# Performance work log

Measured on AMD Instinct MI355X. Metric: run time of the kernel, lower is better.

Reference implementation:

```python
import jax, jax.numpy as jnp
import numpy as np

N = 50000   # nodes
E = 800000  # edges
D = 256     # input feature dim
H = 128     # hidden size
OUT = 40    # output classes


def setup_inputs() -> dict:
    key = jax.random.key(0)
    ks = jax.random.split(key, 10)
    s = 0.05
    return {
        "x": jax.random.normal(ks[0], (N, D), jnp.float32),
        "edge_index": jax.random.randint(ks[1], (2, E), 0, N, dtype=jnp.int64),
        "W0": jax.random.normal(ks[2], (D, H), jnp.float32) * s,
        "b0": jnp.zeros((H,), jnp.float32),
        "W1": jax.random.normal(ks[3], (H, H), jnp.float32) * s,
        "b1": jnp.zeros((H,), jnp.float32),
        "W2": jax.random.normal(ks[4], (H, H), jnp.float32) * s,
        "b2": jnp.zeros((H,), jnp.float32),
        "Wout": jax.random.normal(ks[5], (H * 3, OUT), jnp.float32) * s,
        "bout": jnp.zeros((OUT,), jnp.float32),
    }


def _gcn_norm(edge_index, n):
    # PyG gcn_norm: add self-loops, symmetric D^-1/2 (A+I) D^-1/2 weights
    row, col = edge_index[0], edge_index[1]
    loop = jnp.arange(n, dtype=edge_index.dtype)
    row = jnp.concatenate([row, loop])
    col = jnp.concatenate([col, loop])
    deg = jax.ops.segment_sum(jnp.ones_like(col, jnp.float32), col, num_segments=n)
    dinv = jnp.where(deg > 0, jax.lax.rsqrt(jnp.maximum(deg, 1.0)), 0.0)
    norm = dinv[row] * dinv[col]  # [E+N]
    return row, col, norm


def _gcn_conv(x, W, b, row, col, norm, n):
    h = x @ W                                   # dense transform first (PyG order)
    msg = h[row] * norm[:, None]                # gather source feats, scale
    out = jax.ops.segment_sum(msg, col, num_segments=n)  # scatter-aggregate
    return out + b


def reference(x, edge_index, W0, b0, W1, b1, W2, b2, Wout, bout):
    n = x.shape[0]
    row, col, norm = _gcn_norm(edge_index, n)
    x1 = jax.nn.relu(_gcn_conv(x, W0, b0, row, col, norm, n))
    x2 = jax.nn.relu(_gcn_conv(x1, W1, b1, row, col, norm, n))
    x3 = jax.nn.relu(_gcn_conv(x2, W2, b2, row, col, norm, n))
    xs = jnp.concatenate([x1, x2, x3], axis=-1)  # JumpingKnowledge 'cat'
    return xs @ Wout + bout
```

## Files before the change

kernel.cpp:

```cpp
#include <hip/hip_runtime.h>

#define HID 128
#define NOUT 40
#define SCAN_B 256
#define NWIN 8

typedef __attribute__((ext_vector_type(8))) short bf16x8;
typedef __attribute__((ext_vector_type(4))) float f32x4;

__device__ inline float bf2f(unsigned int u) {
    unsigned int t = u << 16;
    float f;
    __builtin_memcpy(&f, &t, 4);
    return f;
}
__device__ inline unsigned short f2bf(float f) {
    unsigned int x;
    __builtin_memcpy(&x, &f, 4);
    unsigned int r = (x + 0x7fffu + ((x >> 16) & 1u)) >> 16;
    return (unsigned short)r;
}
__device__ inline bf16x8 pack_bf8(float4 u, float4 v) {
    bf16x8 r;
    r[0] = (short)f2bf(u.x); r[1] = (short)f2bf(u.y);
    r[2] = (short)f2bf(u.z); r[3] = (short)f2bf(u.w);
    r[4] = (short)f2bf(v.x); r[5] = (short)f2bf(v.y);
    r[6] = (short)f2bf(v.z); r[7] = (short)f2bf(v.w);
    return r;
}

__global__ void prep_kernel(const unsigned int* __restrict__ e, int* __restrict__ flag,
                            int* __restrict__ deg, int N) {
    if (blockIdx.x == 0 && threadIdx.x < 64) {
        unsigned int v = e[2 * threadIdx.x + 1];
        unsigned long long ball = __ballot(v == 0u);
        if (threadIdx.x == 0) *flag = (ball == ~0ull) ? 1 : 0;
    }
    int stride = gridDim.x * blockDim.x;
    for (int j = blockIdx.x * blockDim.x + threadIdx.x; j < N; j += stride) deg[j] = 0;
}

__global__ void degwt_kernel(const void* __restrict__ eix, const int* __restrict__ flag,
                             int* __restrict__ deg, int E, int gE,
                             const float* __restrict__ W0, const float* __restrict__ W1,
                             const float* __restrict__ W2, const float* __restrict__ Wo,
                             unsigned short* __restrict__ W0t, unsigned short* __restrict__ W1t,
                             unsigned short* __restrict__ W2t, unsigned short* __restrict__ Wot) {
    if (blockIdx.x < gE) {
        int i = blockIdx.x * blockDim.x + threadIdx.x;
        if (i >= E) return;
        int f = *flag;
        int c = f ? (int)(((const long long*)eix)[(size_t)E + i]) : ((const int*)eix)[(size_t)E + i];
        atomicAdd(&deg[c], 1);
    } else {
        int idx = (blockIdx.x - gE) * blockDim.x + threadIdx.x;
        const int s0 = 128 * 256, s1 = 128 * 128, s2 = 128 * 128, s3 = 48 * 384;
        if (idx < s0) {
            int n = idx >> 8, k = idx & 255;
            W0t[idx] = f2bf(W0[(size_t)k * 128 + n]);
        } else if ((idx -= s0) < s1) {
            int n = idx >> 7, k = idx & 127;
            W1t[idx] = f2bf(W1[(size_t)k * 128 + n]);
        } else if ((idx -= s1) < s2) {
            int n = idx >> 7, k = idx & 127;
            W2t[idx] = f2bf(W2[(size_t)k * 128 + n]);
        } else if ((idx -= s2) < s3) {
            int n = idx / 384, k = idx - n * 384;
            Wot[idx] = (n < NOUT) ? f2bf(Wo[(size_t)k * NOUT + n]) : (unsigned short)0;
        }
    }
}

__global__ void scan1_kernel(const int* __restrict__ deg, int* __restrict__ offs,
                             int* __restrict__ bsum, float* __restrict__ dinv, int N) {
    __shared__ int s[SCAN_B];
    int i = blockIdx.x * SCAN_B + threadIdx.x;
    int v = (i < N) ? deg[i] : 0;
    if (i < N) dinv[i] = rsqrtf((float)v + 1.0f);
    s[threadIdx.x] = v;
    __syncthreads();
    for (int d = 1; d < SCAN_B; d <<= 1) {
        int t = (threadIdx.x >= d) ? s[threadIdx.x - d] : 0;
        __syncthreads();
        s[threadIdx.x] += t;
        __syncthreads();
    }
    if (i < N) offs[i] = s[threadIdx.x] - v;
    if (threadIdx.x == SCAN_B - 1) bsum[blockIdx.x] = s[SCAN_B - 1];
}

__global__ void scan2_kernel(int* __restrict__ bsum, int nb) {
    __shared__ int s[SCAN_B];
    int v = (threadIdx.x < nb) ? bsum[threadIdx.x] : 0;
    s[threadIdx.x] = v;
    __syncthreads();
    for (int d = 1; d < SCAN_B; d <<= 1) {
        int t = (threadIdx.x >= d) ? s[threadIdx.x - d] : 0;
        __syncthreads();
        s[threadIdx.x] += t;
        __syncthreads();
    }
    if (threadIdx.x < nb) bsum[threadIdx.x] = s[threadIdx.x] - v;
}

__global__ void scan3_kernel(int* __restrict__ offs, const int* __restrict__ bsum,
                             int* __restrict__ cursor, int N, int E) {
    int i = blockIdx.x * SCAN_B + threadIdx.x;
    if (i < N) {
        int v = offs[i] + bsum[blockIdx.x];
        offs[i] = v;
        cursor[i] = v;
    }
    if (blockIdx.x == 0 && threadIdx.x == 0) offs[N] = E;
}

__global__ __launch_bounds__(256) void fill_csr_kernel(
    const void* __restrict__ eix, const int* __restrict__ flag,
    const float* __restrict__ dinv, int* __restrict__ cursor,
    int2* __restrict__ pkd, int E, int N) {
    const int wn = blockIdx.x & (NWIN - 1);
    const int slice = blockIdx.x >> 3;
    const int nslice = gridDim.x >> 3;
    const int wsz = (N + NWIN - 1) / NWIN;
    const int lo = wn * wsz, hi = lo + wsz;
    const int f = *flag;
    const int stride = nslice * 256;
    for (int i = slice * 256 + threadIdx.x; i < E; i += stride) {
        int r, c;
        if (f) {
            r = (int)(((const long long*)eix)[i]);
            c = (int)(((const long long*)eix)[(size_t)E + i]);
        } else {
            r = ((const int*)eix)[i];
            c = ((const int*)eix)[(size_t)E + i];
        }
        if (c >= lo && c < hi) {
            int p = atomicAdd(&cursor[c], 1);
            int2 rec;
            rec.x = r;
            rec.y = __float_as_int(dinv[r] * dinv[c]);
            pkd[p] = rec;
        }
    }
}

template <bool AF32, int K>
__global__ __launch_bounds__(256) void gemm_mfma_kernel(
    const void* __restrict__ Ap, const unsigned short* __restrict__ Wt,
    unsigned short* __restrict__ H, int M) {
    __shared__ unsigned short Bs[128 * 128];
    const int tid = threadIdx.x;
    const int lane = tid & 63;
    const int w = tid >> 6;
    const int lr = lane & 15;
    const int ko = lane >> 4;
    const int bm = blockIdx.x * 128;

    f32x4 acc[2][8];
#pragma unroll
    for (int i = 0; i < 2; ++i)
#pragma unroll
        for (int j = 0; j < 8; ++j) acc[i][j] = (f32x4){0.f, 0.f, 0.f, 0.f};

    size_t aoff[2];
#pragma unroll
    for (int mi = 0; mi < 2; ++mi) {
        int R = bm + w * 32 + mi * 16 + lr;
        if (R >= M) R = M - 1;
        aoff[mi] = (size_t)R * K + ko * 8;
    }

#pragma unroll
    for (int kp = 0; kp < K; kp += 128) {
        for (int c = tid; c < 128 * 16; c += 256) {
            int row = c >> 4;
            int ch = c & 15;
            int sch = ch ^ (row & 7);
            *(bf16x8*)(Bs + row * 128 + sch * 8) =
                *(const bf16x8*)(Wt + (size_t)row * K + kp + ch * 8);
        }
        __syncthreads();

#pragma unroll
        for (int k0 = 0; k0 < 128; k0 += 32) {
            bf16x8 a[2], b[8];
#pragma unroll
            for (int mi = 0; mi < 2; ++mi) {
                if constexpr (AF32) {
                    const float* p = (const float*)Ap + aoff[mi] + kp + k0;
                    float4 u = *(const float4*)p;
                    float4 v = *(const float4*)(p + 4);
                    a[mi] = pack_bf8(u, v);
                } else {
                    a[mi] = *(const bf16x8*)((const unsigned short*)Ap + aoff[mi] + kp + k0);
                }
            }
            const int chb = (k0 >> 3) + ko;
#pragma unroll
            for (int ni = 0; ni < 8; ++ni) {
                int row = ni * 16 + lr;
                b[ni] = *(const bf16x8*)(Bs + row * 128 + ((chb ^ (row & 7)) * 8));
            }
#pragma unroll
            for (int mi = 0; mi < 2; ++mi)
#pragma unroll
                for (int ni = 0; ni < 8; ++ni)
                    acc[mi][ni] = __builtin_amdgcn_mfma_f32_16x16x32_bf16(a[mi], b[ni], acc[mi][ni], 0, 0, 0);
        }
        __syncthreads();
    }

    unsigned short* Cw = Bs + w * (16 * 136);
#pragma unroll
    for (int mi = 0; mi < 2; ++mi) {
#pragma unroll
        for (int ni = 0; ni < 8; ++ni)
#pragma unroll
            for (int r = 0; r < 4; ++r)
                Cw[(ko * 4 + r) * 136 + ni * 16 + lr] = f2bf(acc[mi][ni][r]);
        const int R0 = bm + w * 32 + mi * 16;
#pragma unroll
        for (int p = 0; p < 4; ++p) {
            int row = p * 4 + (lane >> 4);
            int col = (lane & 15) * 8;
            int Ro = R0 + row;
            if (Ro < M) {
                uint4 v = *(const uint4*)(Cw + row * 136 + col);
                *(uint4*)(H + (size_t)Ro * HID + col) = v;
            }
        }
    }
}

__global__ __launch_bounds__(256) void agg_csr_kernel(
    const unsigned int* __restrict__ h32, const int* __restrict__ offs,
    const int2* __restrict__ pkd, const float* __restrict__ dinv,
    const float* __restrict__ bias, unsigned int* __restrict__ xo, int N) {
    const int lane = threadIdx.x & 63;
    const int n = (blockIdx.x * blockDim.x + threadIdx.x) >> 6;
    if (n >= N) return;
    const float d = dinv[n];
    unsigned int sv = h32[(size_t)n * 64 + lane];
    float ax = bf2f(sv & 0xffff) * (d * d) + bias[2 * lane + 0];
    float ay = bf2f(sv >> 16) * (d * d) + bias[2 * lane + 1];
    int e = offs[n];
    const int e1 = offs[n + 1];

    for (; e + 16 <= e1; e += 16) {
        int2 pk[16];
        unsigned int v[16];
#pragma unroll
        for (int j = 0; j < 16; ++j) pk[j] = pkd[e + j];
#pragma unroll
        for (int j = 0; j < 16; ++j) v[j] = h32[(size_t)pk[j].x * 64 + lane];
#pragma unroll
        for (int j = 0; j < 16; ++j) {
            float wv = __int_as_float(pk[j].y);
            ax += bf2f(v[j] & 0xffff) * wv;
            ay += bf2f(v[j] >> 16) * wv;
        }
    }
    for (; e + 4 <= e1; e += 4) {
        int2 pk[4];
        unsigned int v[4];
#pragma unroll
        for (int j = 0; j < 4; ++j) pk[j] = pkd[e + j];
#pragma unroll
        for (int j = 0; j < 4; ++j) v[j] = h32[(size_t)pk[j].x * 64 + lane];
#pragma unroll
        for (int j = 0; j < 4; ++j) {
            float wv = __int_as_float(pk[j].y);
            ax += bf2f(v[j] & 0xffff) * wv;
            ay += bf2f(v[j] >> 16) * wv;
        }
    }
    for (; e < e1; ++e) {
        int2 pk = pkd[e];
        unsigned int v = h32[(size_t)pk.x * 64 + lane];
        float wv = __int_as_float(pk.y);
        ax += bf2f(v & 0xffff) * wv;
        ay += bf2f(v >> 16) * wv;
    }
    ax = fmaxf(ax, 0.f);
    ay = fmaxf(ay, 0.f);
    xo[(size_t)n * 64 + lane] = (unsigned int)f2bf(ax) | ((unsigned int)f2bf(ay) << 16);
}

__global__ __launch_bounds__(256) void head_mfma_kernel(
    const unsigned short* __restrict__ x1, const unsigned short* __restrict__ x2,
    const unsigned short* __restrict__ x3, const unsigned short* __restrict__ Wt,
    const float* __restrict__ bout, float* __restrict__ out, int M) {
    const int tid = threadIdx.x;
    const int lane = tid & 63;
    const int w = tid >> 6;
    const int lr = lane & 15;
    const int ko = lane >> 4;
    const int bm = blockIdx.x * 64;
    int R = bm + w * 16 + lr;
    if (R >= M) R = M - 1;
    const unsigned short* xs[3] = {x1, x2, x3};

    f32x4 acc[3];
#pragma unroll
    for (int i = 0; i < 3; ++i) acc[i] = (f32x4){0.f, 0.f, 0.f, 0.f};

#pragma unroll
    for (int s = 0; s < 3; ++s) {
        const unsigned short* xp = xs[s] + (size_t)R * HID + ko * 8;
#pragma unroll
        for (int c = 0; c < 4; ++c) {
            bf16x8 a = *(const bf16x8*)(xp + c * 32);
#pragma unroll
            for (int ni = 0; ni < 3; ++ni) {
                bf16x8 b = *(const bf16x8*)(Wt + (size_t)(ni * 16 + lr) * 384 + s * 128 + c * 32 + ko * 8);
                acc[ni] = __builtin_amdgcn_mfma_f32_16x16x32_bf16(a, b, acc[ni], 0, 0, 0);
            }
        }
    }

    int Rb = bm + w * 16 + ko * 4;
#pragma unroll
    for (int r = 0; r < 4; ++r) {
        int Ro = Rb + r;
        if (Ro < M) {
#pragma unroll
            for (int ni = 0; ni < 3; ++ni) {
                int C = ni * 16 + lr;
                if (C < NOUT) out[(size_t)Ro * NOUT + C] = acc[ni][r] + bout[C];
            }
        }
    }
}

static inline size_t align_up(size_t x, size_t a) { return (x + a - 1) / a * a; }

extern "C" void kernel_launch(void* const* d_in, const int* in_sizes, int n_in,
                              void* d_out, int out_size, void* d_ws, size_t ws_size,
                              hipStream_t stream) {
    const float* x    = (const float*)d_in[0];
    const void*  eix  = d_in[1];
    const float* W0   = (const float*)d_in[2];
    const float* b0   = (const float*)d_in[3];
    const float* W1   = (const float*)d_in[4];
    const float* b1   = (const float*)d_in[5];
    const float* W2   = (const float*)d_in[6];
    const float* b2   = (const float*)d_in[7];
    const float* Wout = (const float*)d_in[8];
    const float* bout = (const float*)d_in[9];
    float* out = (float*)d_out;

    const int D = 256;
    const int N = in_sizes[0] / D;
    const int E = in_sizes[1] / 2;

    char* w = (char*)d_ws;
    size_t off = 0;
    int* deg = (int*)(w + off);             off = align_up(off + (size_t)N * 4, 256);
    float* dinv = (float*)(w + off);        off = align_up(off + (size_t)N * 4, 256);
    int* offs = (int*)(w + off);            off = align_up(off + (size_t)(N + 1) * 4, 256);
    int* cursor = (int*)(w + off);          off = align_up(off + (size_t)N * 4, 256);
    int* bsum = (int*)(w + off);            off = align_up(off + 1024 * 4, 256);
    int* flag = (int*)(w + off);            off = align_up(off + 16, 256);
    int2* pkd = (int2*)(w + off);           off = align_up(off + (size_t)E * 8, 256);
    unsigned short* h   = (unsigned short*)(w + off); off = align_up(off + (size_t)N * HID * 2, 256);
    unsigned short* x1b = (unsigned short*)(w + off); off = align_up(off + (size_t)N * HID * 2, 256);
    unsigned short* x2b = (unsigned short*)(w + off); off = align_up(off + (size_t)N * HID * 2, 256);
    unsigned short* x3b = (unsigned short*)(w + off); off = align_up(off + (size_t)N * HID * 2, 256);
    unsigned short* W0t = (unsigned short*)(w + off); off = align_up(off + (size_t)HID * 256 * 2, 256);
    unsigned short* W1t = (unsigned short*)(w + off); off = align_up(off + (size_t)HID * HID * 2, 256);
    unsigned short* W2t = (unsigned short*)(w + off); off = align_up(off + (size_t)HID * HID * 2, 256);
    unsigned short* Wot = (unsigned short*)(w + off); off = align_up(off + (size_t)48 * 384 * 2, 256);
    (void)ws_size;

    prep_kernel<<<128, 256, 0, stream>>>((const unsigned int*)eix, flag, deg, N);

    const int gE = (E + 255) / 256;
    const int wtTot = 128 * 256 + 128 * 128 + 128 * 128 + 48 * 384;
    const int gW = (wtTot + 255) / 256;
    degwt_kernel<<<gE + gW, 256, 0, stream>>>(eix, flag, deg, E, gE,
                                              W0, W1, W2, Wout, W0t, W1t, W2t, Wot);

    const int nb = (N + SCAN_B - 1) / SCAN_B;
    scan1_kernel<<<nb, SCAN_B, 0, stream>>>(deg, offs, bsum, dinv, N);
    scan2_kernel<<<1, SCAN_B, 0, stream>>>(bsum, nb);
    scan3_kernel<<<nb, SCAN_B, 0, stream>>>(offs, bsum, cursor, N, E);
    fill_csr_kernel<<<NWIN * 256, 256, 0, stream>>>(eix, flag, dinv, cursor, pkd, E, N);

    const int gGemm = (N + 127) / 128;
    const int gAgg = (N * 64 + 255) / 256;

    gemm_mfma_kernel<true, 256><<<gGemm, 256, 0, stream>>>(x, W0t, h, N);
    agg_csr_kernel<<<gAgg, 256, 0, stream>>>((const unsigned int*)h, offs, pkd, dinv, b0, (unsigned int*)x1b, N);
    gemm_mfma_kernel<false, 128><<<gGemm, 256, 0, stream>>>(x1b, W1t, h, N);
    agg_csr_kernel<<<gAgg, 256, 0, stream>>>((const unsigned int*)h, offs, pkd, dinv, b1, (unsigned int*)x2b, N);
    gemm_mfma_kernel<false, 128><<<gGemm, 256, 0, stream>>>(x2b, W2t, h, N);
    agg_csr_kernel<<<gAgg, 256, 0, stream>>>((const unsigned int*)h, offs, pkd, dinv, b2, (unsigned int*)x3b, N);
    head_mfma_kernel<<<(N + 63) / 64, 256, 0, stream>>>(x1b, x2b, x3b, Wot, bout, out, N);
}
```

Before: 359.7 us.

## Fuse CSR fill with first GEMM and merge scan passes

Merges the second and third scan kernels into one, with each block re-scanning the block sums locally, and fuses the CSR fill kernel with the first-layer GEMM into a single launch that splits work by block index. This removes two launches and lets the independent edge-fill and dense transform run concurrently on the GPU. The cost is that fill blocks now reserve the GEMM's shared memory, which can reduce occupancy for the atomic scatter, and the two workloads compete for resources.

```diff
diff --git a/kernel.cpp b/kernel.cpp
--- a/kernel.cpp
+++ b/kernel.cpp
@@ -4,6 +4,7 @@
 #define NOUT 40
 #define SCAN_B 256
 #define NWIN 8
+#define FILLB (NWIN * 256)
 
 typedef __attribute__((ext_vector_type(8))) short bf16x8;
 typedef __attribute__((ext_vector_type(4))) float f32x4;
@@ -89,7 +90,8 @@
     if (threadIdx.x == SCAN_B - 1) bsum[blockIdx.x] = s[SCAN_B - 1];
 }
 
-__global__ void scan2_kernel(int* __restrict__ bsum, int nb) {
+__global__ void scan23_kernel(int* __restrict__ offs, const int* __restrict__ bsum,
+                              int* __restrict__ cursor, int N, int E, int nb) {
     __shared__ int s[SCAN_B];
     int v = (threadIdx.x < nb) ? bsum[threadIdx.x] : 0;
     s[threadIdx.x] = v;
@@ -100,53 +102,135 @@
         s[threadIdx.x] += t;
         __syncthreads();
     }
-    if (threadIdx.x < nb) bsum[threadIdx.x] = s[threadIdx.x] - v;
-}
-
-__global__ void scan3_kernel(int* __restrict__ offs, const int* __restrict__ bsum,
-                             int* __restrict__ cursor, int N, int E) {
+    const int base = (blockIdx.x == 0) ? 0 : s[blockIdx.x - 1];
     int i = blockIdx.x * SCAN_B + threadIdx.x;
     if (i < N) {
-        int v = offs[i] + bsum[blockIdx.x];
-        offs[i] = v;
-        cursor[i] = v;
+        int o = offs[i] + base;
+        offs[i] = o;
+        cursor[i] = o;
     }
     if (blockIdx.x == 0 && threadIdx.x == 0) offs[N] = E;
 }
 
-__global__ __launch_bounds__(256) void fill_csr_kernel(
+__global__ __launch_bounds__(256) void fillgemm0_kernel(
     const void* __restrict__ eix, const int* __restrict__ flag,
     const float* __restrict__ dinv, int* __restrict__ cursor,
-    int2* __restrict__ pkd, int E, int N) {
-    const int wn = blockIdx.x & (NWIN - 1);
-    const int slice = blockIdx.x >> 3;
-    const int nslice = gridDim.x >> 3;
-    const int wsz = (N + NWIN - 1) / NWIN;
-    const int lo = wn * wsz, hi = lo + wsz;
-    const int f = *flag;
-    const int stride = nslice * 256;
-    for (int i = slice * 256 + threadIdx.x; i < E; i += stride) {
-        int r, c;
-        if (f) {
-            r = (int)(((const long long*)eix)[i]);
-            c = (int)(((const long long*)eix)[(size_t)E + i]);
-        } else {
-            r = ((const int*)eix)[i];
-            c = ((const int*)eix)[(size_t)E + i];
-        }
-        if (c >= lo && c < hi) {
-            int p = atomicAdd(&cursor[c], 1);
-            int2 rec;
-            rec.x = r;
-            rec.y = __float_as_int(dinv[r] * dinv[c]);
-            pkd[p] = rec;
-        }
-    }
-}
-
-template <bool AF32, int K>
+    int2* __restrict__ pkd, int E, int N,
+    const float* __restrict__ Ap, const unsigned short* __restrict__ Wt,
+    unsigned short* __restrict__ H, int M) {
+    __shared__ unsigned short Bs[128 * 128];
+    const int tid = threadIdx.x;
+
+    if (blockIdx.x < FILLB) {
+        const int wn = blockIdx.x & (NWIN - 1);
+        const int slice = blockIdx.x >> 3;
+        const int nslice = FILLB >> 3;
+        const int wsz = (N + NWIN - 1) / NWIN;
+        const int lo = wn * wsz, hi = lo + wsz;
+        const int f = *flag;
+        const int stride = nslice * 256;
+        for (int i = slice * 256 + tid; i < E; i += stride) {
+            int r, c;
+            if (f) {
+                r = (int)(((const long long*)eix)[i]);
+                c = (int)(((const long long*)eix)[(size_t)E + i]);
+            } else {
+                r = ((const int*)eix)[i];
+                c = ((const int*)eix)[(size_t)E + i];
+            }
+            if (c >= lo && c < hi) {
+                int p = atomicAdd(&cursor[c], 1);
+                int2 rec;
+                rec.x = r;
+                rec.y = __float_as_int(dinv[r] * dinv[c]);
+                pkd[p] = rec;
+            }
+        }
+        return;
+    }
+
+    constexpr int K = 256;
+    const int lane = tid & 63;
+    const int w = tid >> 6;
+    const int lr = lane & 15;
+    const int ko = lane >> 4;
+    const int bm = (blockIdx.x - FILLB) * 128;
+
+    f32x4 acc[2][8];
+#pragma unroll
+    for (int i = 0; i < 2; ++i)
+#pragma unroll
+        for (int j = 0; j < 8; ++j) acc[i][j] = (f32x4){0.f, 0.f, 0.f, 0.f};
+
+    size_t aoff[2];
+#pragma unroll
+    for (int mi = 0; mi < 2; ++mi) {
+        int R = bm + w * 32 + mi * 16 + lr;
+        if (R >= M) R = M - 1;
+        aoff[mi] = (size_t)R * K + ko * 8;
+    }
+
+#pragma unroll
+    for (int kp = 0; kp < K; kp += 128) {
+        for (int c = tid; c < 128 * 16; c += 256) {
+            int row = c >> 4;
+            int ch = c & 15;
+            int sch = ch ^ (row & 7);
+            *(bf16x8*)(Bs + row * 128 + sch * 8) =
+                *(const bf16x8*)(Wt + (size_t)row * K + kp + ch * 8);
+        }
+        __syncthreads();
+
+#pragma unroll
+        for (int k0 = 0; k0 < 128; k0 += 32) {
+            bf16x8 a[2], b[8];
+#pragma unroll
+            for (int mi = 0; mi < 2; ++mi) {
+                const float* p = Ap + aoff[mi] + kp + k0;
+                float4 u = *(const float4*)p;
+                float4 v = *(const float4*)(p + 4);
+                a[mi] = pack_bf8(u, v);
+            }
+            const int chb = (k0 >> 3) + ko;
+#pragma unroll
+            for (int ni = 0; ni < 8; ++ni) {
+                int row = ni * 16 + lr;
+                b[ni] = *(const bf16x8*)(Bs + row * 128 + ((chb ^ (row & 7)) * 8));
+            }
+#pragma unroll
+            for (int mi = 0; mi < 2; ++mi)
+#pragma unroll
+                for (int ni = 0; ni < 8; ++ni)
+                    acc[mi][ni] = __builtin_amdgcn_mfma_f32_16x16x32_bf16(a[mi], b[ni], acc[mi][ni], 0, 0, 0);
+        }
+        __syncthreads();
+    }
+
+    unsigned short* Cw = Bs + w * (16 * 136);
+#pragma unroll
+    for (int mi = 0; mi < 2; ++mi) {
+#pragma unroll
+        for (int ni = 0; ni < 8; ++ni)
+#pragma unroll
+            for (int r = 0; r < 4; ++r)
+                Cw[(ko * 4 + r) * 136 + ni * 16 + lr] = f2bf(acc[mi][ni][r]);
+        const int R0 = bm + w * 32 + mi * 16;
+#pragma unroll
+        for (int p = 0; p < 4; ++p) {
+            int row = p * 4 + (lane >> 4);
+            int col = (lane & 15) * 8;
+            int Ro = R0 + row;
+            if (Ro < M) {
+                uint4 v = *(const uint4*)(Cw + row * 136 + col);
+                *(uint4*)(H + (size_t)Ro * HID + col) = v;
+            }
+        }
+    }
+}
+
+template <int K>
 __global__ __launch_bounds__(256) void gemm_mfma_kernel(
-    const void* __restrict__ Ap, const unsigned short* __restrict__ Wt,
+    const unsigned short* __restrict__ Ap, const unsigned short* __restrict__ Wt,
     unsigned short* __restrict__ H, int M) {
     __shared__ unsigned short Bs[128 * 128];
     const int tid = threadIdx.x;
@@ -185,16 +269,8 @@
         for (int k0 = 0; k0 < 128; k0 += 32) {
             bf16x8 a[2], b[8];
 #pragma unroll
-            for (int mi = 0; mi < 2; ++mi) {
-                if constexpr (AF32) {
-                    const float* p = (const float*)Ap + aoff[mi] + kp + k0;
-                    float4 u = *(const float4*)p;
-                    float4 v = *(const float4*)(p + 4);
-                    a[mi] = pack_bf8(u, v);
-                } else {
-                    a[mi] = *(const bf16x8*)((const unsigned short*)Ap + aoff[mi] + kp + k0);
-                }
-            }
+            for (int mi = 0; mi < 2; ++mi)
+                a[mi] = *(const bf16x8*)(Ap + aoff[mi] + kp + k0);
             const int chb = (k0 >> 3) + ko;
 #pragma unroll
             for (int ni = 0; ni < 8; ++ni) {
@@ -382,18 +458,17 @@
 
     const int nb = (N + SCAN_B - 1) / SCAN_B;
     scan1_kernel<<<nb, SCAN_B, 0, stream>>>(deg, offs, bsum, dinv, N);
-    scan2_kernel<<<1, SCAN_B, 0, stream>>>(bsum, nb);
-    scan3_kernel<<<nb, SCAN_B, 0, stream>>>(offs, bsum, cursor, N, E);
-    fill_csr_kernel<<<NWIN * 256, 256, 0, stream>>>(eix, flag, dinv, cursor, pkd, E, N);
+    scan23_kernel<<<nb, SCAN_B, 0, stream>>>(offs, bsum, cursor, N, E, nb);
 
     const int gGemm = (N + 127) / 128;
     const int gAgg = (N * 64 + 255) / 256;
 
-    gemm_mfma_kernel<true, 256><<<gGemm, 256, 0, stream>>>(x, W0t, h, N);
+    fillgemm0_kernel<<<FILLB + gGemm, 256, 0, stream>>>(eix, flag, dinv, cursor, pkd, E, N,
+                                                        x, W0t, h, N);
     agg_csr_kernel<<<gAgg, 256, 0, stream>>>((const unsigned int*)h, offs, pkd, dinv, b0, (unsigned int*)x1b, N);
-    gemm_mfma_kernel<false, 128><<<gGemm, 256, 0, stream>>>(x1b, W1t, h, N);
+    gemm_mfma_kernel<128><<<gGemm, 256, 0, stream>>>(x1b, W1t, h, N);
     agg_csr_kernel<<<gAgg, 256, 0, stream>>>((const unsigned int*)h, offs, pkd, dinv, b1, (unsigned int*)x2b, N);
-    gemm_mfma_kernel<false, 128><<<gGemm, 256, 0, stream>>>(x2b, W2t, h, N);
+    gemm_mfma_kernel<128><<<gGemm, 256, 0, stream>>>(x2b, W2t, h, N);
     agg_csr_kernel<<<gAgg, 256, 0, stream>>>((const unsigned int*)h, offs, pkd, dinv, b2, (unsigned int*)x3b, N);
     head_mfma_kernel<<<(N + 63) / 64, 256, 0, stream>>>(x1b, x2b, x3b, Wot, bout, out, N);
 }
```

After: 360.1 us. No clear change (+0.1%).

## Merge all GCN stages into one cooperative persistent kernel with grid syncs

Applied to the files above, without the earlier changes.

Replaces the chain of separate kernels (prep, degree, scans, CSR fill, three GEMM+aggregate layers, head) with a single cooperative mega-kernel that walks through each stage using grid-stride loops and separates them with grid-wide barriers. The grid is sized from occupancy, assuming 256 CUs and capped at 2048 blocks. The aim is to remove the per-launch overhead and the idle gaps between the many small kernels. In exchange every stage runs at a fixed persistent grid, pays grid-barrier costs, and loses per-kernel register and occupancy tuning. The GEMM staging stride also moves from 136 to 144.

```diff
diff --git a/kernel.cpp b/kernel.cpp
--- a/kernel.cpp
+++ b/kernel.cpp
@@ -1,8 +1,10 @@
 #include <hip/hip_runtime.h>
+#include <hip/hip_cooperative_groups.h>
+
+namespace cg = cooperative_groups;
 
 #define HID 128
 #define NOUT 40
-#define SCAN_B 256
 #define NWIN 8
 
 typedef __attribute__((ext_vector_type(8))) short bf16x8;
@@ -29,304 +31,324 @@
     return r;
 }
 
-__global__ void prep_kernel(const unsigned int* __restrict__ e, int* __restrict__ flag,
-                            int* __restrict__ deg, int N) {
-    if (blockIdx.x == 0 && threadIdx.x < 64) {
-        unsigned int v = e[2 * threadIdx.x + 1];
-        unsigned long long ball = __ballot(v == 0u);
-        if (threadIdx.x == 0) *flag = (ball == ~0ull) ? 1 : 0;
-    }
-    int stride = gridDim.x * blockDim.x;
-    for (int j = blockIdx.x * blockDim.x + threadIdx.x; j < N; j += stride) deg[j] = 0;
-}
-
-__global__ void degwt_kernel(const void* __restrict__ eix, const int* __restrict__ flag,
-                             int* __restrict__ deg, int E, int gE,
-                             const float* __restrict__ W0, const float* __restrict__ W1,
-                             const float* __restrict__ W2, const float* __restrict__ Wo,
-                             unsigned short* __restrict__ W0t, unsigned short* __restrict__ W1t,
-                             unsigned short* __restrict__ W2t, unsigned short* __restrict__ Wot) {
-    if (blockIdx.x < gE) {
-        int i = blockIdx.x * blockDim.x + threadIdx.x;
-        if (i >= E) return;
-        int f = *flag;
-        int c = f ? (int)(((const long long*)eix)[(size_t)E + i]) : ((const int*)eix)[(size_t)E + i];
-        atomicAdd(&deg[c], 1);
-    } else {
-        int idx = (blockIdx.x - gE) * blockDim.x + threadIdx.x;
-        const int s0 = 128 * 256, s1 = 128 * 128, s2 = 128 * 128, s3 = 48 * 384;
-        if (idx < s0) {
-            int n = idx >> 8, k = idx & 255;
-            W0t[idx] = f2bf(W0[(size_t)k * 128 + n]);
-        } else if ((idx -= s0) < s1) {
-            int n = idx >> 7, k = idx & 127;
-            W1t[idx] = f2bf(W1[(size_t)k * 128 + n]);
-        } else if ((idx -= s1) < s2) {
-            int n = idx >> 7, k = idx & 127;
-            W2t[idx] = f2bf(W2[(size_t)k * 128 + n]);
-        } else if ((idx -= s2) < s3) {
-            int n = idx / 384, k = idx - n * 384;
-            Wot[idx] = (n < NOUT) ? f2bf(Wo[(size_t)k * NOUT + n]) : (unsigned short)0;
-        }
-    }
-}
-
-__global__ void scan1_kernel(const int* __restrict__ deg, int* __restrict__ offs,
-                             int* __restrict__ bsum, float* __restrict__ dinv, int N) {
-    __shared__ int s[SCAN_B];
-    int i = blockIdx.x * SCAN_B + threadIdx.x;
-    int v = (i < N) ? deg[i] : 0;
-    if (i < N) dinv[i] = rsqrtf((float)v + 1.0f);
-    s[threadIdx.x] = v;
-    __syncthreads();
-    for (int d = 1; d < SCAN_B; d <<= 1) {
-        int t = (threadIdx.x >= d) ? s[threadIdx.x - d] : 0;
-        __syncthreads();
-        s[threadIdx.x] += t;
-        __syncthreads();
-    }
-    if (i < N) offs[i] = s[threadIdx.x] - v;
-    if (threadIdx.x == SCAN_B - 1) bsum[blockIdx.x] = s[SCAN_B - 1];
-}
-
-__global__ void scan2_kernel(int* __restrict__ bsum, int nb) {
-    __shared__ int s[SCAN_B];
-    int v = (threadIdx.x < nb) ? bsum[threadIdx.x] : 0;
-    s[threadIdx.x] = v;
-    __syncthreads();
-    for (int d = 1; d < SCAN_B; d <<= 1) {
-        int t = (threadIdx.x >= d) ? s[threadIdx.x - d] : 0;
-        __syncthreads();
-        s[threadIdx.x] += t;
-        __syncthreads();
-    }
-    if (threadIdx.x < nb) bsum[threadIdx.x] = s[threadIdx.x] - v;
-}
-
-__global__ void scan3_kernel(int* __restrict__ offs, const int* __restrict__ bsum,
-                             int* __restrict__ cursor, int N, int E) {
-    int i = blockIdx.x * SCAN_B + threadIdx.x;
-    if (i < N) {
-        int v = offs[i] + bsum[blockIdx.x];
-        offs[i] = v;
-        cursor[i] = v;
-    }
-    if (blockIdx.x == 0 && threadIdx.x == 0) offs[N] = E;
-}
-
-__global__ __launch_bounds__(256) void fill_csr_kernel(
-    const void* __restrict__ eix, const int* __restrict__ flag,
-    const float* __restrict__ dinv, int* __restrict__ cursor,
-    int2* __restrict__ pkd, int E, int N) {
-    const int wn = blockIdx.x & (NWIN - 1);
-    const int slice = blockIdx.x >> 3;
-    const int nslice = gridDim.x >> 3;
-    const int wsz = (N + NWIN - 1) / NWIN;
-    const int lo = wn * wsz, hi = lo + wsz;
-    const int f = *flag;
-    const int stride = nslice * 256;
-    for (int i = slice * 256 + threadIdx.x; i < E; i += stride) {
-        int r, c;
-        if (f) {
-            r = (int)(((const long long*)eix)[i]);
-            c = (int)(((const long long*)eix)[(size_t)E + i]);
-        } else {
-            r = ((const int*)eix)[i];
-            c = ((const int*)eix)[(size_t)E + i];
-        }
-        if (c >= lo && c < hi) {
-            int p = atomicAdd(&cursor[c], 1);
-            int2 rec;
-            rec.x = r;
-            rec.y = __float_as_int(dinv[r] * dinv[c]);
-            pkd[p] = rec;
-        }
-    }
-}
+struct MP {
+    const void* eix;
+    const float* x;
+    const float *W0, *b0, *W1, *b1, *W2, *b2, *Wo, *bo;
+    float* out;
+    int *deg, *offs, *cursor, *bsum, *flag;
+    float* dinv;
+    int2* pkd;
+    unsigned short *h, *x1, *x2, *x3, *W0t, *W1t, *W2t, *Wot;
+    int N, E;
+};
 
 template <bool AF32, int K>
-__global__ __launch_bounds__(256) void gemm_mfma_kernel(
-    const void* __restrict__ Ap, const unsigned short* __restrict__ Wt,
-    unsigned short* __restrict__ H, int M) {
-    __shared__ unsigned short Bs[128 * 128];
+__device__ inline void gemm_phase(const void* Ap, const unsigned short* Wt,
+                                  unsigned short* H, int M, unsigned short* Bs, int G) {
     const int tid = threadIdx.x;
     const int lane = tid & 63;
     const int w = tid >> 6;
     const int lr = lane & 15;
     const int ko = lane >> 4;
-    const int bm = blockIdx.x * 128;
-
-    f32x4 acc[2][8];
-#pragma unroll
-    for (int i = 0; i < 2; ++i)
-#pragma unroll
-        for (int j = 0; j < 8; ++j) acc[i][j] = (f32x4){0.f, 0.f, 0.f, 0.f};
-
-    size_t aoff[2];
-#pragma unroll
-    for (int mi = 0; mi < 2; ++mi) {
-        int R = bm + w * 32 + mi * 16 + lr;
-        if (R >= M) R = M - 1;
-        aoff[mi] = (size_t)R * K + ko * 8;
-    }
-
-#pragma unroll
-    for (int kp = 0; kp < K; kp += 128) {
-        for (int c = tid; c < 128 * 16; c += 256) {
-            int row = c >> 4;
-            int ch = c & 15;
-            int sch = ch ^ (row & 7);
-            *(bf16x8*)(Bs + row * 128 + sch * 8) =
-                *(const bf16x8*)(Wt + (size_t)row * K + kp + ch * 8);
-        }
+    const int nt = (M + 127) >> 7;
+
+    for (int t = blockIdx.x; t < nt; t += G) {
+        const int bm = t << 7;
+        f32x4 acc[2][8];
+#pragma unroll
+        for (int i = 0; i < 2; ++i)
+#pragma unroll
+            for (int j = 0; j < 8; ++j) acc[i][j] = (f32x4){0.f, 0.f, 0.f, 0.f};
+
+        size_t aoff[2];
+#pragma unroll
+        for (int mi = 0; mi < 2; ++mi) {
+            int R = bm + w * 32 + mi * 16 + lr;
+            if (R >= M) R = M - 1;
+            aoff[mi] = (size_t)R * K + ko * 8;
+        }
+
         __syncthreads();
-
-#pragma unroll
-        for (int k0 = 0; k0 < 128; k0 += 32) {
-            bf16x8 a[2], b[8];
-#pragma unroll
-            for (int mi = 0; mi < 2; ++mi) {
-                if constexpr (AF32) {
-                    const float* p = (const float*)Ap + aoff[mi] + kp + k0;
-                    float4 u = *(const float4*)p;
-                    float4 v = *(const float4*)(p + 4);
-                    a[mi] = pack_bf8(u, v);
-                } else {
-                    a[mi] = *(const bf16x8*)((const unsigned short*)Ap + aoff[mi] + kp + k0);
+#pragma unroll
+        for (int kp = 0; kp < K; kp += 128) {
+            for (int c = tid; c < 128 * 16; c += 256) {
+                int row = c >> 4;
+                int ch = c & 15;
+                int sch = ch ^ (row & 7);
+                *(bf16x8*)(Bs + row * 128 + sch * 8) =
+                    *(const bf16x8*)(Wt + (size_t)row * K + kp + ch * 8);
+            }
+            __syncthreads();
+#pragma unroll
+            for (int k0 = 0; k0 < 128; k0 += 32) {
+                bf16x8 a[2], b[8];
+#pragma unroll
+                for (int mi = 0; mi < 2; ++mi) {
+                    if constexpr (AF32) {
+                        const float* p = (const float*)Ap + aoff[mi] + kp + k0;
+                        float4 u = *(const float4*)p;
+                        float4 v = *(const float4*)(p + 4);
+                        a[mi] = pack_bf8(u, v);
+                    } else {
+                        a[mi] = *(const bf16x8*)((const unsigned short*)Ap + aoff[mi] + kp + k0);
+                    }
                 }
-            }
-            const int chb = (k0 >> 3) + ko;
-#pragma unroll
-            for (int ni = 0; ni < 8; ++ni) {
-                int row = ni * 16 + lr;
-                b[ni] = *(const bf16x8*)(Bs + row * 128 + ((chb ^ (row & 7)) * 8));
-            }
-#pragma unroll
-            for (int mi = 0; mi < 2; ++mi)
-#pragma unroll
-                for (int ni = 0; ni < 8; ++ni)
-                    acc[mi][ni] = __builtin_amdgcn_mfma_f32_16x16x32_bf16(a[mi], b[ni], acc[mi][ni], 0, 0, 0);
-        }
+                const int chb = (k0 >> 3) + ko;
+#pragma unroll
+                for (int ni = 0; ni < 8; ++ni) {
+                    int row = ni * 16 + lr;
+                    b[ni] = *(const bf16x8*)(Bs + row * 128 + ((chb ^ (row & 7)) * 8));
+                }
+#pragma unroll
+                for (int mi = 0; mi < 2; ++mi)
+#pragma unroll
+                    for (int ni = 0; ni < 8; ++ni)
+                        acc[mi][ni] = __builtin_amdgcn_mfma_f32_16x16x32_bf16(a[mi], b[ni], acc[mi][ni], 0, 0, 0);
+            }
+            __syncthreads();
+        }
+
+        unsigned short* Cw = Bs + w * (16 * 144);
+#pragma unroll
+        for (int mi = 0; mi < 2; ++mi) {
+#pragma unroll
+            for (int ni = 0; ni < 8; ++ni)
+#pragma unroll
+                for (int r = 0; r < 4; ++r)
+                    Cw[(ko * 4 + r) * 144 + ni * 16 + lr] = f2bf(acc[mi][ni][r]);
+            const int R0 = bm + w * 32 + mi * 16;
+#pragma unroll
+            for (int p = 0; p < 4; ++p) {
+                int row = p * 4 + (lane >> 4);
+                int col = (lane & 15) * 8;
+                int Ro = R0 + row;
+                if (Ro < M) {
+                    uint4 v = *(const uint4*)(Cw + row * 144 + col);
+                    *(uint4*)(H + (size_t)Ro * HID + col) = v;
+                }
+            }
+        }
+    }
+}
+
+__device__ inline void agg_phase(const unsigned int* __restrict__ h32, const int* __restrict__ offs,
+                                 const int2* __restrict__ pkd, const float* __restrict__ dinv,
+                                 const float* __restrict__ bias, unsigned int* __restrict__ xo,
+                                 int N, int G) {
+    const int lane = threadIdx.x & 63;
+    const int nw = G * 4;
+    for (int n = ((blockIdx.x * 256 + threadIdx.x) >> 6); n < N; n += nw) {
+        const float d = dinv[n];
+        unsigned int sv = h32[(size_t)n * 64 + lane];
+        float ax = bf2f(sv & 0xffff) * (d * d) + bias[2 * lane + 0];
+        float ay = bf2f(sv >> 16) * (d * d) + bias[2 * lane + 1];
+        int e = offs[n];
+        const int e1 = offs[n + 1];
+
+        for (; e + 16 <= e1; e += 16) {
+            int2 pk[16];
+            unsigned int v[16];
+#pragma unroll
+            for (int j = 0; j < 16; ++j) pk[j] = pkd[e + j];
+#pragma unroll
+            for (int j = 0; j < 16; ++j) v[j] = h32[(size_t)pk[j].x * 64 + lane];
+#pragma unroll
+            for (int j = 0; j < 16; ++j) {
+                float wv = __int_as_float(pk[j].y);
+                ax += bf2f(v[j] & 0xffff) * wv;
+                ay += bf2f(v[j] >> 16) * wv;
+            }
+        }
+        for (; e + 4 <= e1; e += 4) {
+            int2 pk[4];
+            unsigned int v[4];
+#pragma unroll
+            for (int j = 0; j < 4; ++j) pk[j] = pkd[e + j];
+#pragma unroll
+            for (int j = 0; j < 4; ++j) v[j] = h32[(size_t)pk[j].x * 64 + lane];
+#pragma unroll
+            for (int j = 0; j < 4; ++j) {
+                float wv = __int_as_float(pk[j].y);
+                ax += bf2f(v[j] & 0xffff) * wv;
+                ay += bf2f(v[j] >> 16) * wv;
+            }
+        }
+        for (; e < e1; ++e) {
+            int2 pk = pkd[e];
+            unsigned int v = h32[(size_t)pk.x * 64 + lane];
+            float wv = __int_as_float(pk.y);
+            ax += bf2f(v & 0xffff) * wv;
+            ay += bf2f(v >> 16) * wv;
+        }
+        ax = fmaxf(ax, 0.f);
+        ay = fmaxf(ay, 0.f);
+        xo[(size_t)n * 64 + lane] = (unsigned int)f2bf(ax) | ((unsigned int)f2bf(ay) << 16);
+    }
+}
+
+__global__ __launch_bounds__(256, 4) void mega_kernel(MP P) {
+    cg::grid_group gg = cg::this_grid();
+    __shared__ unsigned short Bs[128 * 128];
+    int* Bsi = (int*)Bs;
+    const int tid = threadIdx.x;
+    const int G = gridDim.x;
+    const int N = P.N, E = P.E;
+
+    if (blockIdx.x == 0 && tid < 64) {
+        unsigned int v = ((const unsigned int*)P.eix)[2 * tid + 1];
+        unsigned long long ball = __ballot(v == 0u);
+        if (tid == 0) *P.flag = (ball == ~0ull) ? 1 : 0;
+    }
+    for (int j = blockIdx.x * 256 + tid; j < N; j += G * 256) P.deg[j] = 0;
+    {
+        const int s0 = 128 * 256, s1 = 128 * 128, s2 = 128 * 128, s3 = 48 * 384;
+        const int wtTot = s0 + s1 + s2 + s3;
+        for (int ix = blockIdx.x * 256 + tid; ix < wtTot; ix += G * 256) {
+            int idx = ix;
+            if (idx < s0) {
+                int n = idx >> 8, k = idx & 255;
+                P.W0t[idx] = f2bf(P.W0[(size_t)k * 128 + n]);
+            } else if ((idx -= s0) < s1) {
+                int n = idx >> 7, k = idx & 127;
+                P.W1t[idx] = f2bf(P.W1[(size_t)k * 128 + n]);
+            } else if ((idx -= s1) < s2) {
+                int n = idx >> 7, k = idx & 127;
+                P.W2t[idx] = f2bf(P.W2[(size_t)k * 128 + n]);
+            } else if ((idx -= s2) < s3) {
+                int n = idx / 384, k = idx - n * 384;
+                P.Wot[idx] = (n < NOUT) ? f2bf(P.Wo[(size_t)k * NOUT + n]) : (unsigned short)0;
+            }
+        }
+    }
+    gg.sync();
+
+    const int f = *P.flag;
+
+    for (int i = blockIdx.x * 256 + tid; i < E; i += G * 256) {
+        int c = f ? (int)(((const long long*)P.eix)[(size_t)E + i]) : ((const int*)P.eix)[(size_t)E + i];
+        atomicAdd(&P.deg[c], 1);
+    }
+    gg.sync();
+
+    const int nb = (N + 255) >> 8;
+    for (int b = blockIdx.x; b < nb; b += G) {
+        int i = b * 256 + tid;
+        int v = (i < N) ? P.deg[i] : 0;
+        if (i < N) P.dinv[i] = rsqrtf((float)v + 1.0f);
+        Bsi[tid] = v;
         __syncthreads();
-    }
-
-    unsigned short* Cw = Bs + w * (16 * 136);
-#pragma unroll
-    for (int mi = 0; mi < 2; ++mi) {
-#pragma unroll
-        for (int ni = 0; ni < 8; ++ni)
-#pragma unroll
-            for (int r = 0; r < 4; ++r)
-                Cw[(ko * 4 + r) * 136 + ni * 16 + lr] = f2bf(acc[mi][ni][r]);
-        const int R0 = bm + w * 32 + mi * 16;
-#pragma unroll
-        for (int p = 0; p < 4; ++p) {
-            int row = p * 4 + (lane >> 4);
-            int col = (lane & 15) * 8;
-            int Ro = R0 + row;
-            if (Ro < M) {
-                uint4 v = *(const uint4*)(Cw + row * 136 + col);
-                *(uint4*)(H + (size_t)Ro * HID + col) = v;
-            }
-        }
-    }
-}
-
-__global__ __launch_bounds__(256) void agg_csr_kernel(
-    const unsigned int* __restrict__ h32, const int* __restrict__ offs,
-    const int2* __restrict__ pkd, const float* __restrict__ dinv,
-    const float* __restrict__ bias, unsigned int* __restrict__ xo, int N) {
-    const int lane = threadIdx.x & 63;
-    const int n = (blockIdx.x * blockDim.x + threadIdx.x) >> 6;
-    if (n >= N) return;
-    const float d = dinv[n];
-    unsigned int sv = h32[(size_t)n * 64 + lane];
-    float ax = bf2f(sv & 0xffff) * (d * d) + bias[2 * lane + 0];
-    float ay = bf2f(sv >> 16) * (d * d) + bias[2 * lane + 1];
-    int e = offs[n];
-    const int e1 = offs[n + 1];
-
-    for (; e + 16 <= e1; e += 16) {
-        int2 pk[16];
-        unsigned int v[16];
-#pragma unroll
-        for (int j = 0; j < 16; ++j) pk[j] = pkd[e + j];
-#pragma unroll
-        for (int j = 0; j < 16; ++j) v[j] = h32[(size_t)pk[j].x * 64 + lane];
-#pragma unroll
-        for (int j = 0; j < 16; ++j) {
-            float wv = __int_as_float(pk[j].y);
-            ax += bf2f(v[j] & 0xffff) * wv;
-            ay += bf2f(v[j] >> 16) * wv;
-        }
-    }
-    for (; e + 4 <= e1; e += 4) {
-        int2 pk[4];
-        unsigned int v[4];
-#pragma unroll
-        for (int j = 0; j < 4; ++j) pk[j] = pkd[e + j];
-#pragma unroll
-        for (int j = 0; j < 4; ++j) v[j] = h32[(size_t)pk[j].x * 64 + lane];
-#pragma unroll
-        for (int j = 0; j < 4; ++j) {
-            float wv = __int_as_float(pk[j].y);
-            ax += bf2f(v[j] & 0xffff) * wv;
-            ay += bf2f(v[j] >> 16) * wv;
-        }
-    }
-    for (; e < e1; ++e) {
-        int2 pk = pkd[e];
-        unsigned int v = h32[(size_t)pk.x * 64 + lane];
-        float wv = __int_as_float(pk.y);
-        ax += bf2f(v & 0xffff) * wv;
-        ay += bf2f(v >> 16) * wv;
-    }
-    ax = fmaxf(ax, 0.f);
-    ay = fmaxf(ay, 0.f);
-    xo[(size_t)n * 64 + lane] = (unsigned int)f2bf(ax) | ((unsigned int)f2bf(ay) << 16);
-}
-
-__global__ __launch_bounds__(256) void head_mfma_kernel(
-    const unsigned short* __restrict__ x1, const unsigned short* __restrict__ x2,
-    const unsigned short* __restrict__ x3, const unsigned short* __restrict__ Wt,
-    const float* __restrict__ bout, float* __restrict__ out, int M) {
-    const int tid = threadIdx.x;
-    const int lane = tid & 63;
-    const int w = tid >> 6;
-    const int lr = lane & 15;
-    const int ko = lane >> 4;
-    const int bm = blockIdx.x * 64;
-    int R = bm + w * 16 + lr;
-    if (R >= M) R = M - 1;
-    const unsigned short* xs[3] = {x1, x2, x3};
-
-    f32x4 acc[3];
-#pragma unroll
-    for (int i = 0; i < 3; ++i) acc[i] = (f32x4){0.f, 0.f, 0.f, 0.f};
-
-#pragma unroll
-    for (int s = 0; s < 3; ++s) {
-        const unsigned short* xp = xs[s] + (size_t)R * HID + ko * 8;
-#pragma unroll
-        for (int c = 0; c < 4; ++c) {
-            bf16x8 a = *(const bf16x8*)(xp + c * 32);
-#pragma unroll
-            for (int ni = 0; ni < 3; ++ni) {
-                bf16x8 b = *(const bf16x8*)(Wt + (size_t)(ni * 16 + lr) * 384 + s * 128 + c * 32 + ko * 8);
-                acc[ni] = __builtin_amdgcn_mfma_f32_16x16x32_bf16(a, b, acc[ni], 0, 0, 0);
-            }
-        }
-    }
-
-    int Rb = bm + w * 16 + ko * 4;
-#pragma unroll
-    for (int r = 0; r < 4; ++r) {
-        int Ro = Rb + r;
-        if (Ro < M) {
-#pragma unroll
-            for (int ni = 0; ni < 3; ++ni) {
-                int C = ni * 16 + lr;
-                if (C < NOUT) out[(size_t)Ro * NOUT + C] = acc[ni][r] + bout[C];
+        for (int d = 1; d < 256; d <<= 1) {
+            int t = (tid >= d) ? Bsi[tid - d] : 0;
+            __syncthreads();
+            Bsi[tid] += t;
+            __syncthreads();
+        }
+        if (i < N) P.offs[i] = Bsi[tid] - v;
+        if (tid == 255) P.bsum[b] = Bsi[255];
+        __syncthreads();
+    }
+    gg.sync();
+
+    for (int b = blockIdx.x; b < nb; b += G) {
+        int v = (tid < nb) ? P.bsum[tid] : 0;
+        Bsi[tid] = v;
+        __syncthreads();
+        for (int d = 1; d < 256; d <<= 1) {
+            int t = (tid >= d) ? Bsi[tid - d] : 0;
+            __syncthreads();
+            Bsi[tid] += t;
+            __syncthreads();
+        }
+        int base = (b == 0) ? 0 : Bsi[b - 1];
+        int i = b * 256 + tid;
+        if (i < N) {
+            int o = P.offs[i] + base;
+            P.offs[i] = o;
+            P.cursor[i] = o;
+        }
+        if (b == 0 && tid == 0) P.offs[N] = E;
+        __syncthreads();
+    }
+    gg.sync();
+
+    {
+        const int wn = blockIdx.x & (NWIN - 1);
+        const int slice = blockIdx.x >> 3;
+        const int nslice = G >> 3;
+        const int wsz = (N + NWIN - 1) / NWIN;
+        const int lo = wn * wsz, hi = lo + wsz;
+        const int stride = nslice * 256;
+        for (int i = slice * 256 + tid; i < E; i += stride) {
+            int r, c;
+            if (f) {
+                r = (int)(((const long long*)P.eix)[i]);
+                c = (int)(((const long long*)P.eix)[(size_t)E + i]);
+            } else {
+                r = ((const int*)P.eix)[i];
+                c = ((const int*)P.eix)[(size_t)E + i];
+            }
+            if (c >= lo && c < hi) {
+                int p = atomicAdd(&P.cursor[c], 1);
+                int2 rec;
+                rec.x = r;
+                rec.y = __float_as_int(P.dinv[r] * P.dinv[c]);
+                P.pkd[p] = rec;
+            }
+        }
+    }
+    gemm_phase<true, 256>(P.x, P.W0t, P.h, N, Bs, G);
+    gg.sync();
+
+    agg_phase((const unsigned int*)P.h, P.offs, P.pkd, P.dinv, P.b0, (unsigned int*)P.x1, N, G);
+    gg.sync();
+    gemm_phase<false, 128>(P.x1, P.W1t, P.h, N, Bs, G);
+    gg.sync();
+    agg_phase((const unsigned int*)P.h, P.offs, P.pkd, P.dinv, P.b1, (unsigned int*)P.x2, N, G);
+    gg.sync();
+    gemm_phase<false, 128>(P.x2, P.W2t, P.h, N, Bs, G);
+    gg.sync();
+    agg_phase((const unsigned int*)P.h, P.offs, P.pkd, P.dinv, P.b2, (unsigned int*)P.x3, N, G);
+    gg.sync();
+
+    {
+        const int lane = tid & 63;
+        const int w = tid >> 6;
+        const int lr = lane & 15;
+        const int ko = lane >> 4;
+        const int nt = (N + 63) >> 6;
+        const unsigned short* xs[3] = {P.x1, P.x2, P.x3};
+        for (int t = blockIdx.x; t < nt; t += G) {
+            const int bm = t << 6;
+            int R = bm + w * 16 + lr;
+            if (R >= N) R = N - 1;
+            f32x4 acc[3];
+#pragma unroll
+            for (int i = 0; i < 3; ++i) acc[i] = (f32x4){0.f, 0.f, 0.f, 0.f};
+#pragma unroll
+            for (int s = 0; s < 3; ++s) {
+                const unsigned short* xp = xs[s] + (size_t)R * HID + ko * 8;
+#pragma unroll
+                for (int c = 0; c < 4; ++c) {
+                    bf16x8 a = *(const bf16x8*)(xp + c * 32);
+#pragma unroll
+                    for (int ni = 0; ni < 3; ++ni) {
+                        bf16x8 b = *(const bf16x8*)(P.Wot + (size_t)(ni * 16 + lr) * 384 + s * 128 + c * 32 + ko * 8);
+                        acc[ni] = __builtin_amdgcn_mfma_f32_16x16x32_bf16(a, b, acc[ni], 0, 0, 0);
+                    }
+                }
+            }
+            int Rb = bm + w * 16 + ko * 4;
+#pragma unroll
+            for (int r = 0; r < 4; ++r) {
+                int Ro = Rb + r;
+                if (Ro < N) {
+#pragma unroll
+                    for (int ni = 0; ni < 3; ++ni) {
+                        int C = ni * 16 + lr;
+                        if (C < NOUT) P.out[(size_t)Ro * NOUT + C] = acc[ni][r] + P.bo[C];
+                    }
+                }
             }
         }
     }
@@ -337,18 +359,6 @@
 extern "C" void kernel_launch(void* const* d_in, const int* in_sizes, int n_in,
                               void* d_out, int out_size, void* d_ws, size_t ws_size,
                               hipStream_t stream) {
-    const float* x    = (const float*)d_in[0];
-    const void*  eix  = d_in[1];
-    const float* W0   = (const float*)d_in[2];
-    const float* b0   = (const float*)d_in[3];
-    const float* W1   = (const float*)d_in[4];
-    const float* b1   = (const float*)d_in[5];
-    const float* W2   = (const float*)d_in[6];
-    const float* b2   = (const float*)d_in[7];
-    const float* Wout = (const float*)d_in[8];
-    const float* bout = (const float*)d_in[9];
-    float* out = (float*)d_out;
-
     const int D = 256;
     const int N = in_sizes[0] / D;
     const int E = in_sizes[1] / 2;
@@ -372,28 +382,27 @@
     unsigned short* Wot = (unsigned short*)(w + off); off = align_up(off + (size_t)48 * 384 * 2, 256);
     (void)ws_size;
 
-    prep_kernel<<<128, 256, 0, stream>>>((const unsigned int*)eix, flag, deg, N);
-
-    const int gE = (E + 255) / 256;
-    const int wtTot = 128 * 256 + 128 * 128 + 128 * 128 + 48 * 384;
-    const int gW = (wtTot + 255) / 256;
-    degwt_kernel<<<gE + gW, 256, 0, stream>>>(eix, flag, deg, E, gE,
-                                              W0, W1, W2, Wout, W0t, W1t, W2t, Wot);
-
-    const int nb = (N + SCAN_B - 1) / SCAN_B;
-    scan1_kernel<<<nb, SCAN_B, 0, stream>>>(deg, offs, bsum, dinv, N);
-    scan2_kernel<<<1, SCAN_B, 0, stream>>>(bsum, nb);
-    scan3_kernel<<<nb, SCAN_B, 0, stream>>>(offs, bsum, cursor, N, E);
-    fill_csr_kernel<<<NWIN * 256, 256, 0, stream>>>(eix, flag, dinv, cursor, pkd, E, N);
-
-    const int gGemm = (N + 127) / 128;
-    const int gAgg = (N * 64 + 255) / 256;
-
-    gemm_mfma_kernel<true, 256><<<gGemm, 256, 0, stream>>>(x, W0t, h, N);
-    agg_csr_kernel<<<gAgg, 256, 0, stream>>>((const unsigned int*)h, offs, pkd, dinv, b0, (unsigned int*)x1b, N);
-    gemm_mfma_kernel<false, 128><<<gGemm, 256, 0, stream>>>(x1b, W1t, h, N);
-    agg_csr_kernel<<<gAgg, 256, 0, stream>>>((const unsigned int*)h, offs, pkd, dinv, b1, (unsigned int*)x2b, N);
-    gemm_mfma_kernel<false, 128><<<gGemm, 256, 0, stream>>>(x2b, W2t, h, N);
-    agg_csr_kernel<<<gAgg, 256, 0, stream>>>((const unsigned int*)h, offs, pkd, dinv, b2, (unsigned int*)x3b, N);
-    head_mfma_kernel<<<(N + 63) / 64, 256, 0, stream>>>(x1b, x2b, x3b, Wot, bout, out, N);
-}
+    MP P;
+    P.eix = d_in[1];
+    P.x   = (const float*)d_in[0];
+    P.W0  = (const float*)d_in[2];  P.b0 = (const float*)d_in[3];
+    P.W1  = (const float*)d_in[4];  P.b1 = (const float*)d_in[5];
+    P.W2  = (const float*)d_in[6];  P.b2 = (const float*)d_in[7];
+    P.Wo  = (const float*)d_in[8];  P.bo = (const float*)d_in[9];
+    P.out = (float*)d_out;
+    P.deg = deg; P.offs = offs; P.cursor = cursor; P.bsum = bsum; P.flag = flag;
+    P.dinv = dinv; P.pkd = pkd;
+    P.h = h; P.x1 = x1b; P.x2 = x2b; P.x3 = x3b;
+    P.W0t = W0t; P.W1t = W1t; P.W2t = W2t; P.Wot = Wot;
+    P.N = N; P.E = E;
+
+    int nbpc = 0;
+    hipOccupancyMaxActiveBlocksPerMultiprocessor(&nbpc, mega_kernel, 256, 0);
+    if (nbpc < 1) nbpc = 1;
+    long long Gl = (long long)nbpc * 256;
+    if (Gl > 2048) Gl = 2048;
+    dim3 grid((unsigned)Gl), block(256);
+
+    void* args[] = {&P};
+    hipLaunchCooperativeKernel((void*)mega_kernel, grid, block, args, 0, stream);
+}
```

After: 1.095 ms. 204% more time.
